# Optimization experiments

Hardware: AMD Instinct MI355X
Metric: run time of the kernel (lower is better)

Reference implementation:

```python
import jax, jax.numpy as jnp
import numpy as np
from jax import lax


def setup_inputs() -> dict:
    key = jax.random.key(0)
    ks = jax.random.split(key, 6)
    T, B = 256, 256
    V, E, H = 512, 256, 512
    x_seq = jax.random.randint(ks[0], (T, B), 0, V, dtype=jnp.int32)
    emb = jax.random.normal(ks[1], (V, E), dtype=jnp.float32)
    emb = emb.at[1].set(0.0)  # padding_idx=1 row is zero in torch
    W_ih = jax.random.normal(ks[2], (4 * H, E), dtype=jnp.float32) * 0.05
    W_hh = jax.random.normal(ks[3], (4 * H, H), dtype=jnp.float32) * 0.05
    b_ih = jax.random.normal(ks[4], (4 * H,), dtype=jnp.float32) * 0.05
    b_hh = jax.random.normal(ks[5], (4 * H,), dtype=jnp.float32) * 0.05
    return {"x_seq": x_seq, "emb": emb, "W_ih": W_ih, "W_hh": W_hh,
            "b_ih": b_ih, "b_hh": b_hh}


def reference(x_seq, emb, W_ih, W_hh, b_ih, b_hh):
    # x_seq: [T, B] int; emb: [V, E]; W_ih: [4H, E]; W_hh: [4H, H]
    T, B = x_seq.shape
    H = W_hh.shape[1]
    e_seq = emb[x_seq]  # [T, B, E]

    def step(carry, e_t):
        h, c = carry
        gates = e_t @ W_ih.T + b_ih + h @ W_hh.T + b_hh  # [B, 4H]
        i, f, g, o = jnp.split(gates, 4, axis=-1)  # torch LSTMCell gate order
        i = jax.nn.sigmoid(i)
        f = jax.nn.sigmoid(f)
        g = jnp.tanh(g)
        o = jax.nn.sigmoid(o)
        c = f * c + i * g
        h = o * jnp.tanh(c)
        return (h, c), h

    h0 = jnp.zeros((B, H), dtype=emb.dtype)
    c0 = jnp.zeros((B, H), dtype=emb.dtype)
    (h, c), outs = lax.scan(step, (h0, c0), e_seq)
    return outs, h, c
```

## Files before the change

### kernel.cpp

```cpp
#include <hip/hip_runtime.h>

#define TS 256
#define BB 256
#define ED 256
#define HD 512

typedef __bf16 bf16_t;
typedef bf16_t bf16x8 __attribute__((ext_vector_type(8)));
typedef float f32x16 __attribute__((ext_vector_type(16)));
typedef float f32x4_t __attribute__((ext_vector_type(4)));
typedef float f32x2_t __attribute__((ext_vector_type(2)));
typedef unsigned short u16x8 __attribute__((ext_vector_type(8)));
typedef int i32x4 __attribute__((ext_vector_type(4)));
typedef int i32x2 __attribute__((ext_vector_type(2)));

#define HGRP_BYTES 65536
#define HBUF_BYTES 524288
#define EBUF_OFF   1048576

#define L_AE   0
#define L_PB   16384
#define L_BIAS 90112
#define L_TOT  90368

__device__ __forceinline__ unsigned short f2bf(float f) {
  unsigned u = __builtin_bit_cast(unsigned, f);
  u += 0x7FFFu + ((u >> 16) & 1u);
  return (unsigned short)(u >> 16);
}
__device__ __forceinline__ float sigm(float x) {
  return __builtin_amdgcn_rcpf(1.f + __expf(-x));
}
__device__ __forceinline__ float tanhf_(float x) {
  return 1.f - 2.f * __builtin_amdgcn_rcpf(1.f + __expf(2.f * x));
}

__device__ __forceinline__ void store_sc1_x2(void* p, i32x2 v) {
  asm volatile("global_store_dwordx2 %0, %1, off sc1" :: "v"(p), "v"(v) : "memory");
}
__device__ __forceinline__ i32x4 load_sc1_x4_issue(const void* p) {
  i32x4 r;
  asm volatile("global_load_dwordx4 %0, %1, off sc1" : "=v"(r) : "v"(p) : "memory");
  return r;
}
__device__ __forceinline__ i32x4 load_sc0_x4_issue(const void* p) {
  i32x4 r;
  asm volatile("global_load_dwordx4 %0, %1, off sc0" : "=v"(r) : "v"(p) : "memory");
  return r;
}
__device__ __forceinline__ int load_sc1_dw_wait(const void* p) {
  int r;
  asm volatile("global_load_dword %0, %1, off sc1\n\ts_waitcnt vmcnt(0)"
               : "=v"(r) : "v"(p) : "memory");
  return r;
}
__device__ __forceinline__ void fence_vm() {
  asm volatile("s_waitcnt vmcnt(0)" ::: "memory");
}
__device__ __forceinline__ void fence_vm8() {
  asm volatile("s_waitcnt vmcnt(8)" ::: "memory");
}

__global__ void emb2bf_kernel(const float* __restrict__ emb,
                              unsigned short* __restrict__ ebuf) {
  int i = blockIdx.x * 256 + threadIdx.x;
  ebuf[i] = f2bf(emb[i]);
}

__global__ __launch_bounds__(256, 1) void lstm_kernel(
    const int* __restrict__ xs, const float* __restrict__ Wih,
    const float* __restrict__ Whh, const float* __restrict__ bih,
    const float* __restrict__ bhh, char* __restrict__ ws,
    float* __restrict__ out)
{
  __shared__ __align__(128) char lds[L_TOT];
  const int tid  = threadIdx.x;
  const int lane = tid & 63;
  const int wv   = tid >> 6;
  const int bg   = blockIdx.x & 7;
  const int gt   = blockIdx.x >> 3;

  const char* ebuf = ws + EBUF_OFF;

  bf16x8 be[4][2], bhf[8][2];
  {
    const int kl = (lane >> 5) << 3;
    #pragma unroll
    for (int nt = 0; nt < 2; ++nt) {
      const int col = nt*32 + (lane & 31);
      const int gr  = (col >> 4)*HD + gt*16 + (col & 15);
      const float* wa = Wih + (size_t)gr * ED;
      const float* wb = Whh + (size_t)gr * HD;
      #pragma unroll
      for (int ks = 0; ks < 4; ++ks) {
        u16x8 tmp;
        #pragma unroll
        for (int j = 0; j < 8; ++j) tmp[j] = f2bf(wa[64*wv + 16*ks + kl + j]);
        be[ks][nt] = __builtin_bit_cast(bf16x8, tmp);
      }
      #pragma unroll
      for (int ks = 0; ks < 8; ++ks) {
        u16x8 tmp;
        #pragma unroll
        for (int j = 0; j < 8; ++j) tmp[j] = f2bf(wb[128*wv + 16*ks + kl + j]);
        bhf[ks][nt] = __builtin_bit_cast(bf16x8, tmp);
      }
    }
  }
  if (tid < 64) {
    const int gr = (tid >> 4)*HD + gt*16 + (tid & 15);
    *(float*)(lds + L_BIAS + tid*4) = bih[gr] + bhh[gr];
  }

  const int e_hi = tid >> 7, e_rr = (tid >> 2) & 31, e_jj = tid & 3;
  const int cu   = e_hi*8 + 2*e_jj;
  float cr0 = 0.f, cr1 = 0.f;

  {
    i32x4 aev[4];
    #pragma unroll
    for (int i = 0; i < 4; ++i) {
      const int ck = i*64 + lane;
      const int row = ck >> 3, c8 = ck & 7;
      const int xv = xs[bg*32 + row];
      aev[i] = *(const i32x4*)(ebuf + xv*512 + wv*128 + c8*16);
    }
    #pragma unroll
    for (int i = 0; i < 4; ++i) {
      const int ck = i*64 + lane;
      const int row = ck >> 3, c8 = ck & 7;
      *(i32x4*)(lds + L_AE + wv*4096 + row*128 + ((c8*16) ^ ((row & 7) << 4))) = aev[i];
    }
  }

  for (int t = 0; t < TS; ++t) {
    const int p = t & 1;
    const char* hsrc = ws + p*HBUF_BYTES + bg*HGRP_BYTES;

    f32x16 acc0 = {}, acc1 = {};
    #pragma unroll
    for (int ks = 0; ks < 4; ++ks) {
      const int row = lane & 31;
      const int koff = 32*ks + ((lane >> 5) << 4);
      bf16x8 a = *(const bf16x8*)(lds + L_AE + wv*4096 + row*128 +
                                  (koff ^ ((row & 7) << 4)));
      acc0 = __builtin_amdgcn_mfma_f32_32x32x16_bf16(a, be[ks][0], acc0, 0, 0, 0);
      acc1 = __builtin_amdgcn_mfma_f32_32x32x16_bf16(a, be[ks][1], acc1, 0, 0, 0);
    }

    i32x4 hv[16];
    #pragma unroll
    for (int ks = 0; ks < 8; ++ks) {
      const char* a = hsrc + ((wv*8 + ks)*64 + lane)*32;
      hv[ks*2]     = load_sc0_x4_issue(a);
      hv[ks*2 + 1] = load_sc0_x4_issue(a + 16);
    }

    {
      const int tw = t << 16;
      unsigned done = 0;

      #define VC(ksc) do { if (!(done & (1u << (ksc)))) {                        \
        const i32x4 lo = hv[(ksc)*2], hh = hv[(ksc)*2 + 1];                      \
        int bad = (lo.x^tw)|(lo.y^tw)|(lo.z^tw)|(lo.w^tw)|                       \
                  (hh.x^tw)|(hh.y^tw)|(hh.z^tw)|(hh.w^tw);                       \
        if (__all((((unsigned)bad) >> 16) == 0)) {                               \
          i32x4 pk;                                                              \
          pk.x = __builtin_amdgcn_perm((unsigned)lo.y,(unsigned)lo.x,0x05040100u);\
          pk.y = __builtin_amdgcn_perm((unsigned)lo.w,(unsigned)lo.z,0x05040100u);\
          pk.z = __builtin_amdgcn_perm((unsigned)hh.y,(unsigned)hh.x,0x05040100u);\
          pk.w = __builtin_amdgcn_perm((unsigned)hh.w,(unsigned)hh.z,0x05040100u);\
          bf16x8 aa = __builtin_bit_cast(bf16x8, pk);                            \
          acc0 = __builtin_amdgcn_mfma_f32_32x32x16_bf16(aa, bhf[(ksc)][0], acc0, 0,0,0); \
          acc1 = __builtin_amdgcn_mfma_f32_32x32x16_bf16(aa, bhf[(ksc)][1], acc1, 0,0,0); \
          done |= (1u << (ksc));                                                 \
        } } } while (0)

      #define RELOAD_MISSING(LOADFN) do {                                        \
        _Pragma("unroll")                                                        \
        for (int ks = 0; ks < 8; ++ks) {                                         \
          if (!(done & (1u << ks))) {                                            \
            const char* a = hsrc + ((wv*8 + ks)*64 + lane)*32;                   \
            hv[ks*2]     = LOADFN(a);                                            \
            hv[ks*2 + 1] = LOADFN(a + 16);                                       \
          }                                                                      \
        }                                                                        \
        fence_vm();                                                              \
        __builtin_amdgcn_sched_barrier(0);                                       \
      } while (0)

      fence_vm8();
      __builtin_amdgcn_sched_barrier(0);
      VC(0); VC(1); VC(2); VC(3);
      fence_vm();
      __builtin_amdgcn_sched_barrier(0);
      VC(4); VC(5); VC(6); VC(7);

      if (done != 0xFFu) {
        RELOAD_MISSING(load_sc0_x4_issue);
        VC(0); VC(1); VC(2); VC(3); VC(4); VC(5); VC(6); VC(7);
      }
      if (done != 0xFFu) {
        RELOAD_MISSING(load_sc1_x4_issue);
        VC(0); VC(1); VC(2); VC(3); VC(4); VC(5); VC(6); VC(7);
      }

      int it = 0;
      while (done != 0xFFu) {
        if (++it > (1 << 15)) break;
        for (;;) {
          int v = tw;
          if (lane < 8 && !(done & (1u << lane)))
            v = load_sc1_dw_wait(hsrc + (wv*8 + lane)*2048);
          if (__all((((unsigned)(v ^ tw)) >> 16) == 0)) break;
          if (++it > (1 << 15)) break;
        }
        if (it > (1 << 15)) break;
        RELOAD_MISSING(load_sc1_x4_issue);
        VC(0); VC(1); VC(2); VC(3); VC(4); VC(5); VC(6); VC(7);
      }
      #undef RELOAD_MISSING
      #undef VC
    }

    {
      const int c0 = lane & 31, hi4 = (lane >> 5) << 2;
      char* pb = lds + L_PB + p*36864 + wv*9216;
      #pragma unroll
      for (int q = 0; q < 4; ++q) {
        const int r0 = q*8 + hi4;
        f32x4_t v0 = {acc0[q*4], acc0[q*4+1], acc0[q*4+2], acc0[q*4+3]};
        f32x4_t v1 = {acc1[q*4], acc1[q*4+1], acc1[q*4+2], acc1[q*4+3]};
        *(f32x4_t*)(pb + (c0*36 + r0)*4)        = v0;
        *(f32x4_t*)(pb + ((32 + c0)*36 + r0)*4) = v1;
      }
    }
    __syncthreads();

    i32x4 aev[4];
    if (t < TS-1) {
      #pragma unroll
      for (int i = 0; i < 4; ++i) {
        const int ck = i*64 + lane;
        const int row = ck >> 3, c8 = ck & 7;
        const int xv = xs[(t+1)*BB + bg*32 + row];
        aev[i] = *(const i32x4*)(ebuf + xv*512 + wv*128 + c8*16);
      }
    }

    float h0, h1;
    {
      const char* pbb = lds + L_PB + p*36864;
      float a8[8];
      #pragma unroll
      for (int g = 0; g < 4; ++g) {
        f32x2_t bv = *(const f32x2_t*)(lds + L_BIAS + (g*16 + cu)*4);
        float s0 = bv[0], s1 = bv[1];
        #pragma unroll
        for (int pp = 0; pp < 4; ++pp) {
          const char* q = pbb + pp*9216 + ((g*16 + cu)*36 + e_rr)*4;
          s0 += *(const float*)(q);
          s1 += *(const float*)(q + 36*4);
        }
        a8[g*2] = s0; a8[g*2+1] = s1;
      }
      const float i0 = sigm(a8[0]),   i1 = sigm(a8[1]);
      const float f0 = sigm(a8[2]),   f1 = sigm(a8[3]);
      const float g0 = tanhf_(a8[4]), g1 = tanhf_(a8[5]);
      const float o0 = sigm(a8[6]),   o1 = sigm(a8[7]);
      cr0 = f0*cr0 + i0*g0;
      cr1 = f1*cr1 + i1*g1;
      h0 = o0 * tanhf_(cr0);
      h1 = o1 * tanhf_(cr1);
    }

    if (t < TS-1) {
      const int tagw = (t + 1) << 16;
      i32x2 d = { tagw | (int)f2bf(h0), tagw | (int)f2bf(h1) };
      store_sc1_x2(ws + (p^1)*HBUF_BYTES + bg*HGRP_BYTES +
                   (gt*64 + e_hi*32 + e_rr)*32 + e_jj*8, d);
    }
    {
      float* orow = out + ((size_t)t*BB + bg*32 + e_rr)*HD + gt*16 + cu;
      *(f32x2_t*)orow = (f32x2_t){h0, h1};
      if (t == TS-1) {
        float* ho = out + (size_t)TS*BB*HD + (size_t)(bg*32 + e_rr)*HD + gt*16 + cu;
        *(f32x2_t*)ho = (f32x2_t){h0, h1};
        float* cb = ho + BB*HD;
        *(f32x2_t*)cb = (f32x2_t){cr0, cr1};
      }
    }

    if (t < TS-1) {
      #pragma unroll
      for (int i = 0; i < 4; ++i) {
        const int ck = i*64 + lane;
        const int row = ck >> 3, c8 = ck & 7;
        *(i32x4*)(lds + L_AE + wv*4096 + row*128 + ((c8*16) ^ ((row & 7) << 4))) = aev[i];
      }
    }
  }
}

extern "C" void kernel_launch(void* const* d_in, const int* in_sizes, int n_in,
                              void* d_out, int out_size, void* d_ws, size_t ws_size,
                              hipStream_t stream) {
  (void)in_sizes; (void)n_in; (void)out_size; (void)ws_size;
  const int*   xs  = (const int*)d_in[0];
  const float* emb = (const float*)d_in[1];
  const float* Wih = (const float*)d_in[2];
  const float* Whh = (const float*)d_in[3];
  const float* bih = (const float*)d_in[4];
  const float* bhh = (const float*)d_in[5];
  char* ws = (char*)d_ws;

  (void)hipMemsetAsync(ws, 0, HBUF_BYTES, stream);
  emb2bf_kernel<<<512, 256, 0, stream>>>(emb, (unsigned short*)(ws + EBUF_OFF));
  lstm_kernel<<<256, 256, 0, stream>>>(xs, Wih, Whh, bih, bhh, ws, (float*)d_out);
}
```

Before: 602.6 us.

## Replace per-element tag words with XOR-checksum validation of packed h data

The h exchange buffer used to tag every bf16 value with the step number in the upper 16 bits, which needed repacking with perm before each MFMA. Now each dword holds two packed bf16 values, and a second dword stores that data XORed with the step number. Readers check lo^hi==t and feed the loaded data straight to the MFMA, so no repacking is needed. The separate single-dword poll loop is replaced by s_sleep plus a full reload, and the iteration cap is halved. The data and checksum arrive as two separate stores, so correctness depends on the XOR check rejecting torn or stale pairs, and a stale value that happens to match could pass.

New measurement: 631.7 us. +4.8%, slower.

```diff
diff --git a/kernel.cpp b/kernel.cpp
--- a/kernel.cpp
+++ b/kernel.cpp
@@ -35,8 +35,8 @@
   return 1.f - 2.f * __builtin_amdgcn_rcpf(1.f + __expf(2.f * x));
 }
 
-__device__ __forceinline__ void store_sc1_x2(void* p, i32x2 v) {
-  asm volatile("global_store_dwordx2 %0, %1, off sc1" :: "v"(p), "v"(v) : "memory");
+__device__ __forceinline__ void store_sc1_dw(void* p, int v) {
+  asm volatile("global_store_dword %0, %1, off sc1" :: "v"(p), "v"(v) : "memory");
 }
 __device__ __forceinline__ i32x4 load_sc1_x4_issue(const void* p) {
   i32x4 r;
@@ -46,12 +46,6 @@
 __device__ __forceinline__ i32x4 load_sc0_x4_issue(const void* p) {
   i32x4 r;
   asm volatile("global_load_dwordx4 %0, %1, off sc0" : "=v"(r) : "v"(p) : "memory");
-  return r;
-}
-__device__ __forceinline__ int load_sc1_dw_wait(const void* p) {
-  int r;
-  asm volatile("global_load_dword %0, %1, off sc1\n\ts_waitcnt vmcnt(0)"
-               : "=v"(r) : "v"(p) : "memory");
   return r;
 }
 __device__ __forceinline__ void fence_vm() {
@@ -157,20 +151,14 @@
     }
 
     {
-      const int tw = t << 16;
+      const int tw = t;
       unsigned done = 0;
 
       #define VC(ksc) do { if (!(done & (1u << (ksc)))) {                        \
         const i32x4 lo = hv[(ksc)*2], hh = hv[(ksc)*2 + 1];                      \
-        int bad = (lo.x^tw)|(lo.y^tw)|(lo.z^tw)|(lo.w^tw)|                       \
-                  (hh.x^tw)|(hh.y^tw)|(hh.z^tw)|(hh.w^tw);                       \
-        if (__all((((unsigned)bad) >> 16) == 0)) {                               \
-          i32x4 pk;                                                              \
-          pk.x = __builtin_amdgcn_perm((unsigned)lo.y,(unsigned)lo.x,0x05040100u);\
-          pk.y = __builtin_amdgcn_perm((unsigned)lo.w,(unsigned)lo.z,0x05040100u);\
-          pk.z = __builtin_amdgcn_perm((unsigned)hh.y,(unsigned)hh.x,0x05040100u);\
-          pk.w = __builtin_amdgcn_perm((unsigned)hh.w,(unsigned)hh.z,0x05040100u);\
-          bf16x8 aa = __builtin_bit_cast(bf16x8, pk);                            \
+        int bad = (hh.x^lo.x^tw)|(hh.y^lo.y^tw)|(hh.z^lo.z^tw)|(hh.w^lo.w^tw);   \
+        if (__all(bad == 0)) {                                                   \
+          bf16x8 aa = __builtin_bit_cast(bf16x8, lo);                            \
           acc0 = __builtin_amdgcn_mfma_f32_32x32x16_bf16(aa, bhf[(ksc)][0], acc0, 0,0,0); \
           acc1 = __builtin_amdgcn_mfma_f32_32x32x16_bf16(aa, bhf[(ksc)][1], acc1, 0,0,0); \
           done |= (1u << (ksc));                                                 \
@@ -207,15 +195,8 @@
 
       int it = 0;
       while (done != 0xFFu) {
-        if (++it > (1 << 15)) break;
-        for (;;) {
-          int v = tw;
-          if (lane < 8 && !(done & (1u << lane)))
-            v = load_sc1_dw_wait(hsrc + (wv*8 + lane)*2048);
-          if (__all((((unsigned)(v ^ tw)) >> 16) == 0)) break;
-          if (++it > (1 << 15)) break;
-        }
-        if (it > (1 << 15)) break;
+        if (++it > (1 << 14)) break;
+        __builtin_amdgcn_s_sleep(4);
         RELOAD_MISSING(load_sc1_x4_issue);
         VC(0); VC(1); VC(2); VC(3); VC(4); VC(5); VC(6); VC(7);
       }
@@ -275,10 +256,11 @@
     }
 
     if (t < TS-1) {
-      const int tagw = (t + 1) << 16;
-      i32x2 d = { tagw | (int)f2bf(h0), tagw | (int)f2bf(h1) };
-      store_sc1_x2(ws + (p^1)*HBUF_BYTES + bg*HGRP_BYTES +
-                   (gt*64 + e_hi*32 + e_rr)*32 + e_jj*8, d);
+      const int dat = (int)f2bf(h0) | ((int)f2bf(h1) << 16);
+      char* hb = ws + (p^1)*HBUF_BYTES + bg*HGRP_BYTES +
+                 (gt*64 + e_hi*32 + e_rr)*32;
+      store_sc1_dw(hb + e_jj*4,      dat);
+      store_sc1_dw(hb + 16 + e_jj*4, dat ^ (t + 1));
     }
     {
       float* orow = out + ((size_t)t*BB + bg*32 + e_rr)*HD + gt*16 + cu;
```
